# Kernel tuning notes

Hardware: AMD Instinct MI355X
Metric: run time of the kernel (lower is better)

The kernel has to match this reference:

```python
import jax, jax.numpy as jnp
import numpy as np
from functools import partial

B = 131072          # training_size (batch)
D_IN = 100          # init_shape
H = 50              # neurons
T = 100             # dimTimes
DT = 0.01           # dt = 1/100
GAMMA = 0.05        # gamma = 1/20
I0 = 0.12


def setup_inputs() -> dict:
    key = jax.random.key(0)
    ks = jax.random.split(key, 7)
    s = lambda fan_in: 1.0 / np.sqrt(fan_in)
    return {
        "x": jax.random.normal(ks[0], (B, D_IN), dtype=jnp.float32),
        "W0": jax.random.uniform(ks[1], (H, D_IN), jnp.float32, -s(D_IN), s(D_IN)),
        "b0": jax.random.uniform(ks[2], (H,), jnp.float32, -s(D_IN), s(D_IN)),
        "W1": jax.random.uniform(ks[3], (H, H), jnp.float32, -s(H), s(H)),
        "b1": jax.random.uniform(ks[4], (H,), jnp.float32, -s(H), s(H)),
        "W2": jax.random.uniform(ks[5], (T - 1, H), jnp.float32, -s(H), s(H)),
        "b2": jax.random.uniform(ks[6], (T - 1,), jnp.float32, -s(H), s(H)),
    }


def reference(x, W0, b0, W1, b1, W2, b2):
    # 3-layer MLP: 100 -> 50 -> 50 -> 99
    h = jax.nn.relu(x @ W0.T + b0)
    h = jax.nn.relu(h @ W1.T + b1)
    out = h @ W2.T + b2                      # [B, T-1] growth rates per step

    # Euler recurrence: I[:,k] = I[:,k-1] + dt*(out[:,k-1]*I*(1-I) - gamma*I)
    i0 = jnp.full((x.shape[0],), I0, dtype=out.dtype)

    def step(I_prev, o_k):
        I_new = I_prev + DT * (o_k * I_prev * (1.0 - I_prev) - GAMMA * I_prev)
        return I_new, I_new

    _, I_rest = jax.lax.scan(step, i0, out.T)   # I_rest: [T-1, B]
    I = jnp.concatenate([i0[:, None], I_rest.T], axis=1)  # [B, T]
    return I
```

## Files before the change

### kernel.cpp

```cpp
#include <hip/hip_runtime.h>
#include <stdint.h>

#define BB      131072
#define TT      100
#define DT_C    0.01f
#define GAMMA_C 0.05f
#define I0_C    0.12f

typedef short bf16x8 __attribute__((ext_vector_type(8)));
typedef float f32x4  __attribute__((ext_vector_type(4)));

#define F0_U16  0
#define F1_U16  (16*512)
#define F2_U16  (24*512)
#define NFRAG_U16 (38*512)
#define B0_F    9728
#define B1_F    (9728+64)
#define B2_F    (9728+128)

__device__ __host__ __forceinline__ uint16_t f2bf(float x) {
    uint32_t u = __builtin_bit_cast(uint32_t, x);
    return (uint16_t)((u + 0x7fffu + ((u >> 16) & 1u)) >> 16);
}

__global__ void pack_kernel(const float* __restrict__ W0, const float* __restrict__ b0,
                            const float* __restrict__ W1, const float* __restrict__ b1,
                            const float* __restrict__ W2, const float* __restrict__ b2,
                            uint16_t* __restrict__ wsu)
{
    const int gid = blockIdx.x * blockDim.x + threadIdx.x;
    const int gsz = gridDim.x * blockDim.x;
    float* wsf = (float*)wsu;

    for (int idx = gid; idx < NFRAG_U16; idx += gsz) {
        int f = idx >> 9;
        int r = idx & 511;
        int L = r >> 3, j = r & 7;
        int k8 = ((L >> 4) << 3) + j;
        int n16 = L & 15;
        float v = 0.0f;
        if (f < 16) {
            int kc = f >> 2, nt = f & 3;
            int kk = kc * 32 + k8, nn = nt * 16 + n16;
            if (kk < 100 && nn < 50) v = W0[nn * 100 + kk];
        } else if (f < 24) {
            int g = f - 16; int kc = g >> 2, nt = g & 3;
            int kk = kc * 32 + k8, nn = nt * 16 + n16;
            if (kk < 50 && nn < 50) v = W1[nn * 50 + kk];
        } else {
            int g = f - 24; int kc = g / 7, nt = g % 7;
            int kk = kc * 32 + k8, nn = nt * 16 + n16;
            if (kk < 50 && nn < 99) v = W2[nn * 50 + kk];
        }
        wsu[idx] = f2bf(v);
    }
    for (int idx = gid; idx < 64; idx += gsz)  wsf[B0_F + idx] = (idx < 50) ? b0[idx] : 0.0f;
    for (int idx = gid; idx < 64; idx += gsz)  wsf[B1_F + idx] = (idx < 50) ? b1[idx] : 0.0f;
    for (int idx = gid; idx < 112; idx += gsz) wsf[B2_F + idx] = (idx < 99) ? b2[idx] : 0.0f;
}

#define SLAB_F 1856

__global__ __launch_bounds__(256, 2) void net_kernel(
    const float* __restrict__ x,
    const void*  __restrict__ wsv,
    float* __restrict__ out)
{
    __shared__ float lds[4 * SLAB_F];
    const int tid  = threadIdx.x;
    const int wave = tid >> 6, lane = tid & 63;
    const int quad = lane >> 4, l15 = lane & 15;
    float* slabF = lds + wave * SLAB_F;
    uint16_t* h0u = (uint16_t*)slabF;
    uint16_t* h1u = (uint16_t*)slabF + 1408;
    const uint16_t* wsu = (const uint16_t*)wsv;
    const float*    wsf = (const float*)wsv;

    const int row0 = (blockIdx.x * 4 + wave) * 16;

    bf16x8 a0[4];
    {
        const float* xrow = x + (size_t)(row0 + l15) * 100;
        #pragma unroll
        for (int kc = 0; kc < 3; ++kc) {
            const float4 p = *(const float4*)(xrow + kc * 32 + quad * 8);
            const float4 q = *(const float4*)(xrow + kc * 32 + quad * 8 + 4);
            bf16x8 f;
            f[0] = (short)f2bf(p.x); f[1] = (short)f2bf(p.y);
            f[2] = (short)f2bf(p.z); f[3] = (short)f2bf(p.w);
            f[4] = (short)f2bf(q.x); f[5] = (short)f2bf(q.y);
            f[6] = (short)f2bf(q.z); f[7] = (short)f2bf(q.w);
            a0[kc] = f;
        }
        bf16x8 f = {0, 0, 0, 0, 0, 0, 0, 0};
        if (quad == 0) {
            const float4 p = *(const float4*)(xrow + 96);
            f[0] = (short)f2bf(p.x); f[1] = (short)f2bf(p.y);
            f[2] = (short)f2bf(p.z); f[3] = (short)f2bf(p.w);
        }
        a0[3] = f;
    }

    f32x4 acc0[4];
    #pragma unroll
    for (int nt = 0; nt < 4; ++nt) acc0[nt] = (f32x4){0.f, 0.f, 0.f, 0.f};
    #pragma unroll
    for (int kc = 0; kc < 4; ++kc) {
        #pragma unroll
        for (int nt = 0; nt < 4; ++nt) {
            bf16x8 b = ((const bf16x8*)(wsu + F0_U16 + (kc * 4 + nt) * 512))[lane];
            acc0[nt] = __builtin_amdgcn_mfma_f32_16x16x32_bf16(a0[kc], b, acc0[nt], 0, 0, 0);
        }
    }
    #pragma unroll
    for (int nt = 0; nt < 4; ++nt) {
        const int n = nt * 16 + l15;
        const float bias = wsf[B0_F + n];
        #pragma unroll
        for (int r = 0; r < 4; ++r) {
            const int m = quad * 4 + r;
            h0u[m * 88 + n] = f2bf(fmaxf(acc0[nt][r] + bias, 0.0f));
        }
    }
    __syncthreads();

    bf16x8 a1[2];
    #pragma unroll
    for (int kc = 0; kc < 2; ++kc)
        a1[kc] = *(const bf16x8*)(h0u + l15 * 88 + kc * 32 + quad * 8);

    f32x4 acc1[4];
    #pragma unroll
    for (int nt = 0; nt < 4; ++nt) acc1[nt] = (f32x4){0.f, 0.f, 0.f, 0.f};
    #pragma unroll
    for (int kc = 0; kc < 2; ++kc) {
        #pragma unroll
        for (int nt = 0; nt < 4; ++nt) {
            bf16x8 b = ((const bf16x8*)(wsu + F1_U16 + (kc * 4 + nt) * 512))[lane];
            acc1[nt] = __builtin_amdgcn_mfma_f32_16x16x32_bf16(a1[kc], b, acc1[nt], 0, 0, 0);
        }
    }
    #pragma unroll
    for (int nt = 0; nt < 4; ++nt) {
        const int n = nt * 16 + l15;
        const float bias = wsf[B1_F + n];
        #pragma unroll
        for (int r = 0; r < 4; ++r) {
            const int m = quad * 4 + r;
            h1u[m * 88 + n] = f2bf(fmaxf(acc1[nt][r] + bias, 0.0f));
        }
    }
    __syncthreads();

    bf16x8 a2[2];
    #pragma unroll
    for (int kc = 0; kc < 2; ++kc)
        a2[kc] = *(const bf16x8*)(h1u + l15 * 88 + kc * 32 + quad * 8);

    f32x4 acc2[7];
    #pragma unroll
    for (int nt = 0; nt < 7; ++nt) acc2[nt] = (f32x4){0.f, 0.f, 0.f, 0.f};
    #pragma unroll
    for (int kc = 0; kc < 2; ++kc) {
        #pragma unroll
        for (int nt = 0; nt < 7; ++nt) {
            bf16x8 b = ((const bf16x8*)(wsu + F2_U16 + (kc * 7 + nt) * 512))[lane];
            acc2[nt] = __builtin_amdgcn_mfma_f32_16x16x32_bf16(a2[kc], b, acc2[nt], 0, 0, 0);
        }
    }
    __syncthreads();

    #pragma unroll
    for (int nt = 0; nt < 7; ++nt) {
        const int t = nt * 16 + l15;
        if (t < 99) {
            const float bias = wsf[B2_F + t];
            #pragma unroll
            for (int r = 0; r < 4; ++r) {
                const int m = quad * 4 + r;
                slabF[m * 116 + t] = acc2[nt][r] + bias;
            }
        }
    }
    __syncthreads();

    if (lane < 16) {
        float* orow = slabF + lane * 116;
        float prev = I0_C;
        #pragma unroll
        for (int k = 1; k < TT; ++k) {
            const float o = orow[k - 1];
            orow[k - 1] = prev;
            prev = prev + DT_C * (o * prev * (1.0f - prev) - GAMMA_C * prev);
        }
        orow[TT - 1] = prev;
    }
    __syncthreads();

    float* gout = out + (size_t)row0 * 100;
    #pragma unroll
    for (int q2 = 0; q2 < 7; ++q2) {
        const int i = q2 * 64 + lane;
        if (i < 400) {
            const int m = i / 25, c4 = (i % 25) * 4;
            f32x4 v = *(const f32x4*)(slabF + m * 116 + c4);
            *(f32x4*)(gout + 4 * i) = v;
        }
    }
}

extern "C" void kernel_launch(void* const* d_in, const int* in_sizes, int n_in,
                              void* d_out, int out_size, void* d_ws, size_t ws_size,
                              hipStream_t stream) {
    const float* x  = (const float*)d_in[0];
    const float* W0 = (const float*)d_in[1];
    const float* b0 = (const float*)d_in[2];
    const float* W1 = (const float*)d_in[3];
    const float* b1 = (const float*)d_in[4];
    const float* W2 = (const float*)d_in[5];
    const float* b2 = (const float*)d_in[6];
    float* out = (float*)d_out;
    uint16_t* wsu = (uint16_t*)d_ws;

    pack_kernel<<<dim3(80), dim3(256), 0, stream>>>(W0, b0, W1, b1, W2, b2, wsu);
    net_kernel<<<dim3(BB / 64), dim3(256), 0, stream>>>(x, (const void*)wsu, out);
}
```

Measured before the change: 124.3 us.

## Process 32 rows per wave, fold biases into GEMMs, drop block barriers

Each wave now handles two 16-row tiles, so every weight fragment loaded from global memory feeds two MFMAs. Biases are folded into the weight fragments through an augmented constant-one input column, dt is prescaled into W2, and the Euler step is reduced to a single fma and multiply. The __syncthreads calls are removed because each wave only touches its own LDS slab, and the grid is halved. In exchange, LDS per block doubles and register pressure rises, which could reduce occupancy, and the extra bf16 rounding of the biases and scaled W2 may shift numerical results.

```diff
diff --git a/kernel.cpp b/kernel.cpp
--- a/kernel.cpp
+++ b/kernel.cpp
@@ -14,13 +14,14 @@
 #define F1_U16  (16*512)
 #define F2_U16  (24*512)
 #define NFRAG_U16 (38*512)
-#define B0_F    9728
-#define B1_F    (9728+64)
-#define B2_F    (9728+128)
-
-__device__ __host__ __forceinline__ uint16_t f2bf(float x) {
+
+__device__ __forceinline__ uint16_t f2bf(float x) {
     uint32_t u = __builtin_bit_cast(uint32_t, x);
     return (uint16_t)((u + 0x7fffu + ((u >> 16) & 1u)) >> 16);
+}
+
+__device__ __forceinline__ uint32_t pk2(float a, float b) {
+    return (uint32_t)f2bf(a) | ((uint32_t)f2bf(b) << 16);
 }
 
 __global__ void pack_kernel(const float* __restrict__ W0, const float* __restrict__ b0,
@@ -30,8 +31,6 @@
 {
     const int gid = blockIdx.x * blockDim.x + threadIdx.x;
     const int gsz = gridDim.x * blockDim.x;
-    float* wsf = (float*)wsu;
-
     for (int idx = gid; idx < NFRAG_U16; idx += gsz) {
         int f = idx >> 9;
         int r = idx & 511;
@@ -42,24 +41,30 @@
         if (f < 16) {
             int kc = f >> 2, nt = f & 3;
             int kk = kc * 32 + k8, nn = nt * 16 + n16;
-            if (kk < 100 && nn < 50) v = W0[nn * 100 + kk];
+            if (nn < 50) {
+                if (kk < 100) v = W0[nn * 100 + kk];
+                else if (kk == 100) v = b0[nn];
+            }
         } else if (f < 24) {
             int g = f - 16; int kc = g >> 2, nt = g & 3;
             int kk = kc * 32 + k8, nn = nt * 16 + n16;
-            if (kk < 50 && nn < 50) v = W1[nn * 50 + kk];
+            if (nn < 50) {
+                if (kk < 50) v = W1[nn * 50 + kk];
+                else if (kk == 50) v = b1[nn];
+            }
         } else {
             int g = f - 24; int kc = g / 7, nt = g % 7;
             int kk = kc * 32 + k8, nn = nt * 16 + n16;
-            if (kk < 50 && nn < 99) v = W2[nn * 50 + kk];
+            if (nn < 99) {
+                if (kk < 50) v = DT_C * W2[nn * 50 + kk];
+                else if (kk == 50) v = DT_C * b2[nn];
+            }
         }
         wsu[idx] = f2bf(v);
     }
-    for (int idx = gid; idx < 64; idx += gsz)  wsf[B0_F + idx] = (idx < 50) ? b0[idx] : 0.0f;
-    for (int idx = gid; idx < 64; idx += gsz)  wsf[B1_F + idx] = (idx < 50) ? b1[idx] : 0.0f;
-    for (int idx = gid; idx < 112; idx += gsz) wsf[B2_F + idx] = (idx < 99) ? b2[idx] : 0.0f;
-}
-
-#define SLAB_F 1856
+}
+
+#define SLAB_F 3712
 
 __global__ __launch_bounds__(256, 2) void net_kernel(
     const float* __restrict__ x,
@@ -72,136 +77,155 @@
     const int quad = lane >> 4, l15 = lane & 15;
     float* slabF = lds + wave * SLAB_F;
     uint16_t* h0u = (uint16_t*)slabF;
-    uint16_t* h1u = (uint16_t*)slabF + 1408;
+    uint16_t* h1u = (uint16_t*)slabF + 32 * 88;
     const uint16_t* wsu = (const uint16_t*)wsv;
-    const float*    wsf = (const float*)wsv;
-
-    const int row0 = (blockIdx.x * 4 + wave) * 16;
-
-    bf16x8 a0[4];
-    {
-        const float* xrow = x + (size_t)(row0 + l15) * 100;
+
+    const int row0 = (blockIdx.x * 4 + wave) * 32;
+
+    bf16x8 a0[2][4];
+    #pragma unroll
+    for (int h = 0; h < 2; ++h) {
+        const float* xrow = x + (size_t)(row0 + h * 16 + l15) * 100;
         #pragma unroll
         for (int kc = 0; kc < 3; ++kc) {
-            const float4 p = *(const float4*)(xrow + kc * 32 + quad * 8);
-            const float4 q = *(const float4*)(xrow + kc * 32 + quad * 8 + 4);
-            bf16x8 f;
-            f[0] = (short)f2bf(p.x); f[1] = (short)f2bf(p.y);
-            f[2] = (short)f2bf(p.z); f[3] = (short)f2bf(p.w);
-            f[4] = (short)f2bf(q.x); f[5] = (short)f2bf(q.y);
-            f[6] = (short)f2bf(q.z); f[7] = (short)f2bf(q.w);
-            a0[kc] = f;
-        }
-        bf16x8 f = {0, 0, 0, 0, 0, 0, 0, 0};
+            f32x4 p = *(const f32x4*)(xrow + kc * 32 + quad * 8);
+            f32x4 q = *(const f32x4*)(xrow + kc * 32 + quad * 8 + 4);
+            union { bf16x8 v; uint32_t u[4]; } t;
+            t.u[0] = pk2(p[0], p[1]); t.u[1] = pk2(p[2], p[3]);
+            t.u[2] = pk2(q[0], q[1]); t.u[3] = pk2(q[2], q[3]);
+            a0[h][kc] = t.v;
+        }
+        union { bf16x8 v; uint32_t u[4]; } t;
+        t.u[0] = t.u[1] = t.u[2] = t.u[3] = 0u;
         if (quad == 0) {
-            const float4 p = *(const float4*)(xrow + 96);
-            f[0] = (short)f2bf(p.x); f[1] = (short)f2bf(p.y);
-            f[2] = (short)f2bf(p.z); f[3] = (short)f2bf(p.w);
-        }
-        a0[3] = f;
-    }
-
-    f32x4 acc0[4];
-    #pragma unroll
-    for (int nt = 0; nt < 4; ++nt) acc0[nt] = (f32x4){0.f, 0.f, 0.f, 0.f};
+            f32x4 p = *(const f32x4*)(xrow + 96);
+            t.u[0] = pk2(p[0], p[1]); t.u[1] = pk2(p[2], p[3]);
+            t.u[2] = 0x00003f80u;
+        }
+        a0[h][3] = t.v;
+    }
+
+    f32x4 acc0[2][4];
+    #pragma unroll
+    for (int h = 0; h < 2; ++h)
+        #pragma unroll
+        for (int nt = 0; nt < 4; ++nt) acc0[h][nt] = (f32x4){0.f, 0.f, 0.f, 0.f};
     #pragma unroll
     for (int kc = 0; kc < 4; ++kc) {
         #pragma unroll
         for (int nt = 0; nt < 4; ++nt) {
             bf16x8 b = ((const bf16x8*)(wsu + F0_U16 + (kc * 4 + nt) * 512))[lane];
-            acc0[nt] = __builtin_amdgcn_mfma_f32_16x16x32_bf16(a0[kc], b, acc0[nt], 0, 0, 0);
-        }
-    }
-    #pragma unroll
-    for (int nt = 0; nt < 4; ++nt) {
-        const int n = nt * 16 + l15;
-        const float bias = wsf[B0_F + n];
-        #pragma unroll
-        for (int r = 0; r < 4; ++r) {
-            const int m = quad * 4 + r;
-            h0u[m * 88 + n] = f2bf(fmaxf(acc0[nt][r] + bias, 0.0f));
-        }
-    }
-    __syncthreads();
-
-    bf16x8 a1[2];
-    #pragma unroll
-    for (int kc = 0; kc < 2; ++kc)
-        a1[kc] = *(const bf16x8*)(h0u + l15 * 88 + kc * 32 + quad * 8);
-
-    f32x4 acc1[4];
-    #pragma unroll
-    for (int nt = 0; nt < 4; ++nt) acc1[nt] = (f32x4){0.f, 0.f, 0.f, 0.f};
+            acc0[0][nt] = __builtin_amdgcn_mfma_f32_16x16x32_bf16(a0[0][kc], b, acc0[0][nt], 0, 0, 0);
+            acc0[1][nt] = __builtin_amdgcn_mfma_f32_16x16x32_bf16(a0[1][kc], b, acc0[1][nt], 0, 0, 0);
+        }
+    }
+    const bool is50 = (l15 == 2);
+    #pragma unroll
+    for (int h = 0; h < 2; ++h) {
+        #pragma unroll
+        for (int nt = 0; nt < 4; ++nt) {
+            const int n = nt * 16 + l15;
+            #pragma unroll
+            for (int r2 = 0; r2 < 4; r2 += 2) {
+                float v0 = fmaxf(acc0[h][nt][r2], 0.0f);
+                float v1 = fmaxf(acc0[h][nt][r2 + 1], 0.0f);
+                if (nt == 3 && is50) { v0 = 1.0f; v1 = 1.0f; }
+                uint32_t p = pk2(v0, v1);
+                const int m = h * 16 + quad * 4 + r2;
+                h0u[m * 88 + n]       = (uint16_t)p;
+                h0u[(m + 1) * 88 + n] = (uint16_t)(p >> 16);
+            }
+        }
+    }
+
+    bf16x8 a1[2][2];
+    #pragma unroll
+    for (int h = 0; h < 2; ++h)
+        #pragma unroll
+        for (int kc = 0; kc < 2; ++kc)
+            a1[h][kc] = *(const bf16x8*)(h0u + (h * 16 + l15) * 88 + kc * 32 + quad * 8);
+
+    f32x4 acc1[2][4];
+    #pragma unroll
+    for (int h = 0; h < 2; ++h)
+        #pragma unroll
+        for (int nt = 0; nt < 4; ++nt) acc1[h][nt] = (f32x4){0.f, 0.f, 0.f, 0.f};
     #pragma unroll
     for (int kc = 0; kc < 2; ++kc) {
         #pragma unroll
         for (int nt = 0; nt < 4; ++nt) {
             bf16x8 b = ((const bf16x8*)(wsu + F1_U16 + (kc * 4 + nt) * 512))[lane];
-            acc1[nt] = __builtin_amdgcn_mfma_f32_16x16x32_bf16(a1[kc], b, acc1[nt], 0, 0, 0);
-        }
-    }
-    #pragma unroll
-    for (int nt = 0; nt < 4; ++nt) {
-        const int n = nt * 16 + l15;
-        const float bias = wsf[B1_F + n];
-        #pragma unroll
-        for (int r = 0; r < 4; ++r) {
-            const int m = quad * 4 + r;
-            h1u[m * 88 + n] = f2bf(fmaxf(acc1[nt][r] + bias, 0.0f));
-        }
-    }
-    __syncthreads();
-
-    bf16x8 a2[2];
-    #pragma unroll
-    for (int kc = 0; kc < 2; ++kc)
-        a2[kc] = *(const bf16x8*)(h1u + l15 * 88 + kc * 32 + quad * 8);
-
-    f32x4 acc2[7];
-    #pragma unroll
-    for (int nt = 0; nt < 7; ++nt) acc2[nt] = (f32x4){0.f, 0.f, 0.f, 0.f};
+            acc1[0][nt] = __builtin_amdgcn_mfma_f32_16x16x32_bf16(a1[0][kc], b, acc1[0][nt], 0, 0, 0);
+            acc1[1][nt] = __builtin_amdgcn_mfma_f32_16x16x32_bf16(a1[1][kc], b, acc1[1][nt], 0, 0, 0);
+        }
+    }
+    #pragma unroll
+    for (int h = 0; h < 2; ++h) {
+        #pragma unroll
+        for (int nt = 0; nt < 4; ++nt) {
+            const int n = nt * 16 + l15;
+            #pragma unroll
+            for (int r2 = 0; r2 < 4; r2 += 2) {
+                float v0 = fmaxf(acc1[h][nt][r2], 0.0f);
+                float v1 = fmaxf(acc1[h][nt][r2 + 1], 0.0f);
+                if (nt == 3 && is50) { v0 = 1.0f; v1 = 1.0f; }
+                uint32_t p = pk2(v0, v1);
+                const int m = h * 16 + quad * 4 + r2;
+                h1u[m * 88 + n]       = (uint16_t)p;
+                h1u[(m + 1) * 88 + n] = (uint16_t)(p >> 16);
+            }
+        }
+    }
+
+    bf16x8 a2[2][2];
+    #pragma unroll
+    for (int h = 0; h < 2; ++h)
+        #pragma unroll
+        for (int kc = 0; kc < 2; ++kc)
+            a2[h][kc] = *(const bf16x8*)(h1u + (h * 16 + l15) * 88 + kc * 32 + quad * 8);
+
+    f32x4 acc2[2][7];
+    #pragma unroll
+    for (int h = 0; h < 2; ++h)
+        #pragma unroll
+        for (int nt = 0; nt < 7; ++nt) acc2[h][nt] = (f32x4){0.f, 0.f, 0.f, 0.f};
     #pragma unroll
     for (int kc = 0; kc < 2; ++kc) {
         #pragma unroll
         for (int nt = 0; nt < 7; ++nt) {
             bf16x8 b = ((const bf16x8*)(wsu + F2_U16 + (kc * 7 + nt) * 512))[lane];
-            acc2[nt] = __builtin_amdgcn_mfma_f32_16x16x32_bf16(a2[kc], b, acc2[nt], 0, 0, 0);
-        }
-    }
-    __syncthreads();
-
-    #pragma unroll
-    for (int nt = 0; nt < 7; ++nt) {
-        const int t = nt * 16 + l15;
-        if (t < 99) {
-            const float bias = wsf[B2_F + t];
+            acc2[0][nt] = __builtin_amdgcn_mfma_f32_16x16x32_bf16(a2[0][kc], b, acc2[0][nt], 0, 0, 0);
+            acc2[1][nt] = __builtin_amdgcn_mfma_f32_16x16x32_bf16(a2[1][kc], b, acc2[1][nt], 0, 0, 0);
+        }
+    }
+    #pragma unroll
+    for (int h = 0; h < 2; ++h) {
+        #pragma unroll
+        for (int nt = 0; nt < 7; ++nt) {
+            const int t = nt * 16 + l15;
             #pragma unroll
-            for (int r = 0; r < 4; ++r) {
-                const int m = quad * 4 + r;
-                slabF[m * 116 + t] = acc2[nt][r] + bias;
-            }
-        }
-    }
-    __syncthreads();
-
-    if (lane < 16) {
+            for (int r = 0; r < 4; ++r)
+                slabF[(h * 16 + quad * 4 + r) * 116 + t] = acc2[h][nt][r];
+        }
+    }
+
+    if (lane < 32) {
         float* orow = slabF + lane * 116;
         float prev = I0_C;
         #pragma unroll
         for (int k = 1; k < TT; ++k) {
-            const float o = orow[k - 1];
+            const float op = orow[k - 1];
             orow[k - 1] = prev;
-            prev = prev + DT_C * (o * prev * (1.0f - prev) - GAMMA_C * prev);
+            prev = prev * fmaf(op, 1.0f - prev, 1.0f - DT_C * GAMMA_C);
         }
         orow[TT - 1] = prev;
     }
-    __syncthreads();
 
     float* gout = out + (size_t)row0 * 100;
     #pragma unroll
-    for (int q2 = 0; q2 < 7; ++q2) {
-        const int i = q2 * 64 + lane;
-        if (i < 400) {
+    for (int q = 0; q < 13; ++q) {
+        const int i = q * 64 + lane;
+        if (i < 800) {
             const int m = i / 25, c4 = (i % 25) * 4;
             f32x4 v = *(const f32x4*)(slabF + m * 116 + c4);
             *(f32x4*)(gout + 4 * i) = v;
@@ -223,5 +247,5 @@
     uint16_t* wsu = (uint16_t*)d_ws;
 
     pack_kernel<<<dim3(80), dim3(256), 0, stream>>>(W0, b0, W1, b1, W2, b2, wsu);
-    net_kernel<<<dim3(BB / 64), dim3(256), 0, stream>>>(x, (const void*)wsu, out);
-}
+    net_kernel<<<dim3(BB / 128), dim3(256), 0, stream>>>(x, (const void*)wsu, out);
+}
```

Measured after the change: 123.6 us. About the same (-0.5%).
